# Optimization experiments

Measured on AMD Instinct MI355X. Metric: run time of the kernel, lower is better.

Reference implementation:

```python
import jax, jax.numpy as jnp
from jax import lax
import numpy as np

K = 2        # k-hop MIS / number of rw SpGEMM iterations
EPS = 0.5    # lazy random-walk epsilon
N = 2048     # nodes
D = 512      # feature dim
E = 65536    # edges (avg degree 32)


def setup_inputs() -> dict:
    key = jax.random.key(0)
    k1, k2, k3, k4 = jax.random.split(key, 4)
    edge_index = jax.random.randint(k1, (2, E), 0, N, dtype=jnp.int32)
    edge_attr = jax.random.uniform(k2, (E,), dtype=jnp.float32)
    x = jax.random.normal(k3, (N, D), dtype=jnp.float32)
    rank = jnp.arange(N, dtype=jnp.int32)  # node ordering ('random' ordering = some permutation; identity here)
    u = jax.random.uniform(k4, (N, N), dtype=jnp.float32)  # noise for row-wise multinomial sampling
    return {"edge_index": edge_index, "edge_attr": edge_attr, "x": x, "rank": rank, "u": u}


def _maximal_k_independent_set(row, col, rank, n, k):
    """Greedy maximal k-independent set: nodes that are local rank-minima within k hops."""
    big = jnp.int32(n)

    def prop_min(r):  # one hop of min-propagation (message row -> col), keep self
        return jnp.minimum(jax.ops.segment_min(r[row], col, num_segments=n), r)

    def prop_or(b):   # one hop of boolean OR propagation (as int32)
        return jnp.maximum(jax.ops.segment_max(b[row], col, num_segments=n), b)

    def cond(st):
        mis, mask, mr = st
        return ~jnp.all(mask)

    def body(st):
        mis, mask, mr = st
        for _ in range(k):
            mr = prop_min(mr)
        mis = mis | (rank == mr)
        mk = mis.astype(jnp.int32)
        for _ in range(k):
            mk = prop_or(mk)
        mask = mk > 0
        mr = jnp.where(mask, big, rank)
        return mis, mask, mr

    init = (jnp.zeros(n, bool), jnp.zeros(n, bool), rank)
    mis, _, _ = lax.while_loop(cond, body, init)
    return mis


def _row_normalize(m):
    s = m.sum(axis=1, keepdims=True)
    return m / jnp.where(s > 0, s, 1.0)


def reference(edge_index, edge_attr, x, rank, u):
    n = x.shape[0]
    row, col = edge_index[0], edge_index[1]

    # --- MIS over the graph structure (integer-only) ---
    mis = _maximal_k_independent_set(row, col, rank, n, K)

    # --- adjacency (dense padded form of the SparseTensor) ---
    adj = jnp.zeros((n, n), x.dtype).at[row, col].add(edge_attr)

    # --- lazy random walk: rw = D^-1 A, offdiag *= (1-eps), diag = old_diag + eps ---
    rw = _row_normalize(adj)
    di = jnp.arange(n)
    new_diag = rw[di, di] + EPS  # computed BEFORE scaling, per original code
    rw = (rw * (1.0 - EPS)).at[di, di].set(new_diag)

    # --- c_mat = rw^K @ eye[:, mis]; padded to [n, n] with zero non-MIS columns ---
    c = jnp.where(mis[None, :], jnp.eye(n, dtype=x.dtype), 0.0)
    for _ in range(K):
        c = rw @ c
    c = _row_normalize(c)

    # --- sample_partition_matrix: per-row multinomial via Gumbel-argmax ---
    g = -jnp.log(-jnp.log(u + 1e-20) + 1e-20)
    logits = jnp.where(c > 0, jnp.log(jnp.maximum(c, 1e-30)), -jnp.inf) + g
    cluster = jnp.argmax(logits, axis=1)                 # [n] cluster id (a MIS column)
    c_hard = jax.nn.one_hot(cluster, n, dtype=x.dtype)   # partition matrix [n, n]

    # --- p_inv = row-normalized c_hard.T ---
    counts = c_hard.sum(axis=0)
    p_inv = c_hard.T / jnp.where(counts > 0, counts, 1.0)[:, None]

    # --- coarsen: c^T A c, pool: p_inv @ x ---
    adj_c = c_hard.T @ adj @ c_hard
    x_pool = p_inv @ x
    return adj_c, c_hard, p_inv, mis, x_pool
```

## Files before the change

kernel.cpp:

```cpp
#include <hip/hip_runtime.h>
#include <hip/hip_bf16.h>
#include <math.h>
#include <stdint.h>

#define NN 2048
#define DD 512
#define EE 65536
#define EPSV 0.5f
#define SEN 2048
#define PADE 98304

static const size_t SZ = (size_t)NN * NN;

__global__ __launch_bounds__(256) void count_deg(const int* __restrict__ row,
                                                 const int* __restrict__ col,
                                                 int* __restrict__ degree,
                                                 int* __restrict__ cdeg) {
  int e = blockIdx.x * 256 + threadIdx.x;
  atomicAdd(&degree[row[e]], 1);
  atomicAdd(&cdeg[col[e]], 1);
}

__global__ __launch_bounds__(1024) void csr_scan_pad(const int* __restrict__ degree,
                                                     const int* __restrict__ cdeg,
                                                     int* __restrict__ row_ptr,
                                                     int* __restrict__ fill_ptr,
                                                     int* __restrict__ col_ptr,
                                                     int* __restrict__ cfill_ptr,
                                                     unsigned short* __restrict__ colidx,
                                                     unsigned short* __restrict__ rowidx,
                                                     float* __restrict__ avals,
                                                     unsigned long long* __restrict__ packed,
                                                     int* __restrict__ counts) {
  __shared__ int a[NN], b[NN], c[NN], d[NN];
  int t = threadIdx.x;
  for (int v = t; v < NN; v += 1024) {
    a[v] = (degree[v] + 15) & ~15;
    c[v] = (cdeg[v] + 15) & ~15;
    packed[v] = 0ull;
    counts[v] = 0;
  }
  __syncthreads();
  int* s1 = a; int* d1 = b; int* s2 = c; int* d2 = d;
  for (int off = 1; off < NN; off <<= 1) {
    for (int v = t; v < NN; v += 1024) {
      d1[v] = s1[v] + (v >= off ? s1[v - off] : 0);
      d2[v] = s2[v] + (v >= off ? s2[v - off] : 0);
    }
    __syncthreads();
    int* tp = s1; s1 = d1; d1 = tp;
    tp = s2; s2 = d2; d2 = tp;
  }
  for (int v = t; v < NN; v += 1024) {
    int dg = degree[v];
    int end = s1[v];
    int excl = end - ((dg + 15) & ~15);
    row_ptr[v] = excl;
    fill_ptr[v] = excl;
    for (int e = excl + dg; e < end; ++e) {
      colidx[e] = (unsigned short)v;
      avals[e] = 0.f;
    }
    dg = cdeg[v];
    end = s2[v];
    excl = end - ((dg + 15) & ~15);
    col_ptr[v] = excl;
    cfill_ptr[v] = excl;
    for (int e = excl + dg; e < end; ++e) rowidx[e] = (unsigned short)v;
  }
  if (t == 0) {
    row_ptr[NN] = s1[NN - 1];
    col_ptr[NN] = s2[NN - 1];
  }
}

__global__ __launch_bounds__(256) void csr_fill(const int* __restrict__ row,
                                                const int* __restrict__ col,
                                                const float* __restrict__ attr,
                                                int* __restrict__ fill_ptr,
                                                int* __restrict__ cfill_ptr,
                                                unsigned short* __restrict__ colidx,
                                                unsigned short* __restrict__ rowidx,
                                                float* __restrict__ avals) {
  int e = blockIdx.x * 256 + threadIdx.x;
  int r = row[e], c = col[e];
  int pos = atomicAdd(&fill_ptr[r], 1);
  colidx[pos] = (unsigned short)c;
  avals[pos] = attr[e];
  rowidx[atomicAdd(&cfill_ptr[c], 1)] = (unsigned short)r;
}

__global__ __launch_bounds__(1024) void mis_kernel(const int* __restrict__ row_ptr_g,
                                                   const int* __restrict__ col_ptr_g,
                                                   const unsigned short* __restrict__ colidx,
                                                   const unsigned short* __restrict__ rowidx,
                                                   const int* __restrict__ rank_g,
                                                   int* __restrict__ mis_flag,
                                                   int* __restrict__ mis_list,
                                                   int* __restrict__ misinv,
                                                   int* __restrict__ mis_count) {
  __shared__ int rank_s[NN];
  __shared__ int mr[NN];
  __shared__ int cov[NN];
  __shared__ int dly[NN];
  __shared__ int mis_s[NN];
  __shared__ int row_ptr_s[NN + 1];
  __shared__ int col_ptr_s[NN + 1];
  __shared__ int unc[2][NN];
  __shared__ int dl[NN];
  __shared__ int ucnt[2];
  __shared__ int dcnt;
  __shared__ int cnt;
  int t = threadIdx.x;
  const uint4* col4 = (const uint4*)colidx;
  const uint4* row4 = (const uint4*)rowidx;

  for (int v = t; v < NN; v += 1024) {
    int rk = rank_g[v];
    rank_s[v] = rk;
    mr[v] = rk;
    cov[v] = 0;
    dly[v] = 0;
    mis_s[v] = 0;
    row_ptr_s[v] = row_ptr_g[v];
    col_ptr_s[v] = col_ptr_g[v];
    unc[0][v] = v;
  }
  if (t == 0) {
    row_ptr_s[NN] = row_ptr_g[NN];
    col_ptr_s[NN] = col_ptr_g[NN];
    ucnt[0] = NN;
    ucnt[1] = 0;
    dcnt = 0;
    cnt = 0;
  }
  __syncthreads();

  int cur = 0;
  for (int round = 0; round < NN; ++round) {
    int U = ucnt[cur];
    if (round) {
      for (int v = t; v < NN; v += 1024) {
        mr[v] = cov[v] ? SEN : rank_s[v];
        dly[v] = 0;
      }
      if (t == 0) { ucnt[cur ^ 1] = 0; dcnt = 0; }
      __syncthreads();
    }
    for (int i = t; i < U; i += 1024) {
      int v = unc[cur][i];
      int val = rank_s[v];
      int e0 = row_ptr_s[v];
      int nch = (row_ptr_s[v + 1] - e0) >> 3;
      const uint4* b4 = col4 + (e0 >> 3);
      for (int cI = 0; cI < nch; cI += 2) {
        uint4 A = b4[cI], B = b4[cI + 1];
        atomicMin(&mr[A.x & 0xFFFFu], val); atomicMin(&mr[A.x >> 16], val);
        atomicMin(&mr[A.y & 0xFFFFu], val); atomicMin(&mr[A.y >> 16], val);
        atomicMin(&mr[A.z & 0xFFFFu], val); atomicMin(&mr[A.z >> 16], val);
        atomicMin(&mr[A.w & 0xFFFFu], val); atomicMin(&mr[A.w >> 16], val);
        atomicMin(&mr[B.x & 0xFFFFu], val); atomicMin(&mr[B.x >> 16], val);
        atomicMin(&mr[B.y & 0xFFFFu], val); atomicMin(&mr[B.y >> 16], val);
        atomicMin(&mr[B.z & 0xFFFFu], val); atomicMin(&mr[B.z >> 16], val);
        atomicMin(&mr[B.w & 0xFFFFu], val); atomicMin(&mr[B.w >> 16], val);
      }
    }
    __syncthreads();
    for (int i = t; i < U; i += 1024) {
      int v = unc[cur][i];
      int val = mr[v];
      int e0 = col_ptr_s[v];
      int nch = (col_ptr_s[v + 1] - e0) >> 3;
      const uint4* b4 = row4 + (e0 >> 3);
      for (int cI = 0; cI < nch; cI += 2) {
        uint4 A = b4[cI], B = b4[cI + 1];
        int m0 = min(mr[A.x & 0xFFFFu], mr[A.x >> 16]);
        int m1 = min(mr[A.y & 0xFFFFu], mr[A.y >> 16]);
        int m2 = min(mr[A.z & 0xFFFFu], mr[A.z >> 16]);
        int m3 = min(mr[A.w & 0xFFFFu], mr[A.w >> 16]);
        int m4 = min(mr[B.x & 0xFFFFu], mr[B.x >> 16]);
        int m5 = min(mr[B.y & 0xFFFFu], mr[B.y >> 16]);
        int m6 = min(mr[B.z & 0xFFFFu], mr[B.z >> 16]);
        int m7 = min(mr[B.w & 0xFFFFu], mr[B.w >> 16]);
        val = min(val, min(min(min(m0, m1), min(m2, m3)),
                           min(min(m4, m5), min(m6, m7))));
      }
      if (rank_s[v] == val) {
        mis_s[v] = 1;
        dly[v] = 1;
        dl[atomicAdd(&dcnt, 1)] = v;
      }
    }
    __syncthreads();
    int D = dcnt;
    for (int i = t; i < D; i += 1024) {
      int v = dl[i];
      int e0 = row_ptr_s[v];
      int nch = (row_ptr_s[v + 1] - e0) >> 3;
      const uint4* b4 = col4 + (e0 >> 3);
      for (int cI = 0; cI < nch; cI += 2) {
        uint4 A = b4[cI], B = b4[cI + 1];
        dly[A.x & 0xFFFFu] = 1; dly[A.x >> 16] = 1;
        dly[A.y & 0xFFFFu] = 1; dly[A.y >> 16] = 1;
        dly[A.z & 0xFFFFu] = 1; dly[A.z >> 16] = 1;
        dly[A.w & 0xFFFFu] = 1; dly[A.w >> 16] = 1;
        dly[B.x & 0xFFFFu] = 1; dly[B.x >> 16] = 1;
        dly[B.y & 0xFFFFu] = 1; dly[B.y >> 16] = 1;
        dly[B.z & 0xFFFFu] = 1; dly[B.z >> 16] = 1;
        dly[B.w & 0xFFFFu] = 1; dly[B.w >> 16] = 1;
      }
    }
    __syncthreads();
    for (int i = t; i < U; i += 1024) {
      int v = unc[cur][i];
      int c1 = dly[v];
      if (!c1) {
        int e0 = col_ptr_s[v];
        int nch = (col_ptr_s[v + 1] - e0) >> 3;
        const uint4* b4 = row4 + (e0 >> 3);
        for (int cI = 0; cI < nch; cI += 2) {
          uint4 A = b4[cI], B = b4[cI + 1];
          c1 |= dly[A.x & 0xFFFFu] | dly[A.x >> 16] |
                dly[A.y & 0xFFFFu] | dly[A.y >> 16] |
                dly[A.z & 0xFFFFu] | dly[A.z >> 16] |
                dly[A.w & 0xFFFFu] | dly[A.w >> 16] |
                dly[B.x & 0xFFFFu] | dly[B.x >> 16] |
                dly[B.y & 0xFFFFu] | dly[B.y >> 16] |
                dly[B.z & 0xFFFFu] | dly[B.z >> 16] |
                dly[B.w & 0xFFFFu] | dly[B.w >> 16];
          if (c1) break;
        }
      }
      if (c1) cov[v] = 1;
      else unc[cur ^ 1][atomicAdd(&ucnt[cur ^ 1], 1)] = v;
    }
    __syncthreads();
    if (ucnt[cur ^ 1] == 0) break;
    cur ^= 1;
  }

  for (int v = t; v < NN; v += 1024) {
    int s = mis_s[v];
    mis_flag[v] = s;
    int slot = -1;
    if (s) {
      slot = atomicAdd(&cnt, 1);
      mis_list[slot] = v;
    }
    misinv[v] = slot;
  }
  __syncthreads();
  if (t == 0) *mis_count = cnt;
}

__global__ __launch_bounds__(256) void rw_build(const int* __restrict__ row_ptr,
                                                const unsigned short* __restrict__ colidx,
                                                const float* __restrict__ avals,
                                                const int* __restrict__ misinv,
                                                float* __restrict__ rw,
                                                float* __restrict__ Bc) {
  int i = blockIdx.x;
  __shared__ float rowbuf[NN];
  __shared__ float ssum;
  int t = threadIdx.x;
  for (int j = t; j < NN; j += 256) rowbuf[j] = 0.f;
  if (t == 0) ssum = 0.f;
  __syncthreads();
  int e0 = row_ptr[i], e1 = row_ptr[i + 1];
  float part = 0.f;
  for (int e = e0 + t; e < e1; e += 256) {
    float a = avals[e];
    atomicAdd(&rowbuf[colidx[e]], a);
    part += a;
  }
  for (int off = 32; off; off >>= 1) part += __shfl_down(part, off);
  if ((t & 63) == 0) atomicAdd(&ssum, part);
  __syncthreads();
  float s = ssum;
  s = (s > 0.f) ? s : 1.f;
  for (int j = t; j < NN; j += 256) {
    float v = rowbuf[j] / s;
    v = (i == j) ? (v + EPSV) : (v * (1.f - EPSV));
    rw[(size_t)i * NN + j] = v;
    int tc = misinv[j];
    if (tc >= 0) Bc[(size_t)tc * NN + i] = v;
  }
}

__device__ inline unsigned int f32_key(float x) {
  unsigned int u = __float_as_uint(x);
  return (u & 0x80000000u) ? ~u : (u | 0x80000000u);
}
__device__ inline float dot4(float4 a, float4 b) {
  return ((a.x * b.x + a.y * b.y) + (a.z * b.z + a.w * b.w));
}
__device__ inline unsigned long long umax64(unsigned long long a, unsigned long long b) {
  return a > b ? a : b;
}
__device__ inline int pdecode(unsigned long long p) {
  return (p == 0ull) ? 0 : (NN - 1 - (int)(p & 0xFFFFFFFFull));
}

__global__ __launch_bounds__(256) void c2_argmax(const float* __restrict__ rw,
                                                 const float* __restrict__ Bc,
                                                 const float* __restrict__ u,
                                                 const int* __restrict__ mis_list,
                                                 const int* __restrict__ mis_count,
                                                 unsigned long long* __restrict__ packed) {
  int M = *mis_count;
  int ncg = (M + 3) >> 2;
  int njobs = ncg * 64;
  int lane = threadIdx.x & 63, w = threadIdx.x >> 6;
  for (int j = blockIdx.x; j < njobs; j += gridDim.x) {
    int cg = j >> 6, tile = j & 63;
    int c0 = cg * 4;
    float4 creg[4][8];
    int mcol[4];
#pragma unroll
    for (int cc = 0; cc < 4; ++cc) {
      int colv = c0 + cc;
      int cl = colv < M ? colv : (M - 1);
      mcol[cc] = mis_list[cl];
      const float4* cb = (const float4*)(Bc + (size_t)cl * NN);
#pragma unroll
      for (int q = 0; q < 8; ++q) creg[cc][q] = cb[q * 64 + lane];
    }
    int rbase = tile * 32 + w * 8;
#pragma unroll
    for (int it = 0; it < 8; ++it) {
      int r = rbase + it;
      const float4* rp = (const float4*)(rw + (size_t)r * NN);
      float4 a0 = rp[lane], a1 = rp[64 + lane], a2 = rp[128 + lane], a3 = rp[192 + lane];
      float4 a4 = rp[256 + lane], a5 = rp[320 + lane], a6 = rp[384 + lane], a7 = rp[448 + lane];
      float sacc[4];
#pragma unroll
      for (int cc = 0; cc < 4; ++cc) {
        float s01 = dot4(a0, creg[cc][0]) + dot4(a1, creg[cc][1]);
        float s23 = dot4(a2, creg[cc][2]) + dot4(a3, creg[cc][3]);
        float s45 = dot4(a4, creg[cc][4]) + dot4(a5, creg[cc][5]);
        float s67 = dot4(a6, creg[cc][6]) + dot4(a7, creg[cc][7]);
        float s = (s01 + s23) + (s45 + s67);
        s += __shfl_xor(s, 32);
        s += __shfl_xor(s, 16);
        s += __shfl_xor(s, 8);
        s += __shfl_xor(s, 4);
        s += __shfl_xor(s, 2);
        s += __shfl_xor(s, 1);
        sacc[cc] = s;
      }
      if (lane == 0) {
        unsigned long long best = 0ull;
#pragma unroll
        for (int cc = 0; cc < 4; ++cc) {
          if (c0 + cc < M && sacc[cc] > 0.f) {
            int m = mcol[cc];
            float uu = u[(size_t)r * NN + m];
            float g = -logf(-logf(uu + 1e-20f) + 1e-20f);
            float logit = logf(sacc[cc]) + g;
            unsigned long long key =
                ((unsigned long long)f32_key(logit) << 32) | (unsigned int)(NN - 1 - m);
            best = umax64(best, key);
          }
        }
        if (best) atomicMax(&packed[r], best);
      }
    }
  }
}

__global__ __launch_bounds__(256) void decode_zero(const unsigned long long* __restrict__ packed,
                                                   int* __restrict__ cluster,
                                                   int* __restrict__ counts,
                                                   float* __restrict__ adjc,
                                                   float* __restrict__ xp) {
  int idx = blockIdx.x * 256 + threadIdx.x;
  if (idx < (int)SZ) adjc[idx] = 0.f;
  else xp[idx - (int)SZ] = 0.f;
  if (idx < NN) {
    int m = pdecode(packed[idx]);
    cluster[idx] = m;
    atomicAdd(&counts[m], 1);
  }
}

__global__ __launch_bounds__(256) void scatter_chpm(const int* __restrict__ row,
                                                    const int* __restrict__ col,
                                                    const float* __restrict__ attr,
                                                    const float* __restrict__ x,
                                                    const int* __restrict__ cluster,
                                                    const int* __restrict__ counts,
                                                    const int* __restrict__ mis_flag,
                                                    float* __restrict__ out_ch,
                                                    float* __restrict__ out_pinv,
                                                    float* __restrict__ out_mis,
                                                    float* __restrict__ adjc,
                                                    float* __restrict__ xp) {
  int idx = blockIdx.x * 256 + threadIdx.x;
  int a = idx >> 11, b = idx & (NN - 1);
  out_ch[idx] = (cluster[a] == b) ? 1.f : 0.f;
  float pv = 0.f;
  if (cluster[b] == a) {
    int c = counts[a];
    pv = 1.f / (float)(c > 0 ? c : 1);
  }
  out_pinv[idx] = pv;
  if (idx < NN) out_mis[idx] = mis_flag[idx] ? 1.f : 0.f;
  if (idx < NN * DD) {
    int i = idx >> 9;
    int ci = cluster[i];
    int c = counts[ci];
    atomicAdd(&xp[ci * DD + (idx & (DD - 1))], x[idx] / (float)(c > 0 ? c : 1));
  }
  if (idx < EE) {
    atomicAdd(&adjc[(size_t)cluster[row[idx]] * NN + cluster[col[idx]]], attr[idx]);
  }
}

extern "C" void kernel_launch(void* const* d_in, const int* in_sizes, int n_in,
                              void* d_out, int out_size, void* d_ws, size_t ws_size,
                              hipStream_t stream) {
  const int*   edge_index = (const int*)d_in[0];
  const float* edge_attr  = (const float*)d_in[1];
  const float* x          = (const float*)d_in[2];
  const int*   rank       = (const int*)d_in[3];
  const float* u          = (const float*)d_in[4];
  float* out              = (float*)d_out;

  const int* row = edge_index;
  const int* col = edge_index + EE;

  float* out_adjc = out;
  float* out_ch   = out + SZ;
  float* out_pinv = out + 2 * SZ;
  float* out_mis  = out + 3 * SZ;
  float* out_xp   = out + 3 * SZ + NN;

  int*   degree    = (int*)d_ws;
  int*   cdeg      = degree + NN;
  unsigned long long* packed = (unsigned long long*)(cdeg + NN);
  int*   counts    = (int*)(packed + NN);
  int*   mis_flag  = counts + NN;
  int*   cluster   = mis_flag + NN;
  int*   mis_list  = cluster + NN;
  int*   misinv    = mis_list + NN;
  int*   mis_count = misinv + NN;
  int*   fill_ptr  = mis_count + 1;
  int*   cfill_ptr = fill_ptr + NN;
  int*   row_ptr   = cfill_ptr + NN;
  int*   col_ptr   = row_ptr + NN + 1;
  unsigned short* colidx =
      (unsigned short*)(((uintptr_t)(col_ptr + NN + 1) + 31) & ~(uintptr_t)31);
  unsigned short* rowidx = colidx + PADE;
  float* avals = (float*)(rowidx + PADE);

  hipMemsetAsync(d_ws, 0, 2 * NN * sizeof(int), stream);
  count_deg<<<EE / 256, 256, 0, stream>>>(row, col, degree, cdeg);
  csr_scan_pad<<<1, 1024, 0, stream>>>(degree, cdeg, row_ptr, fill_ptr, col_ptr,
                                       cfill_ptr, colidx, rowidx, avals, packed, counts);
  csr_fill<<<EE / 256, 256, 0, stream>>>(row, col, edge_attr, fill_ptr, cfill_ptr,
                                         colidx, rowidx, avals);
  mis_kernel<<<1, 1024, 0, stream>>>(row_ptr, col_ptr, colidx, rowidx, rank,
                                     mis_flag, mis_list, misinv, mis_count);
  rw_build<<<NN, 256, 0, stream>>>(row_ptr, colidx, avals, misinv, out_adjc, out_ch);
  c2_argmax<<<1024, 256, 0, stream>>>(out_adjc, out_ch, u, mis_list, mis_count, packed);
  decode_zero<<<(unsigned)((SZ + (size_t)NN * DD) / 256), 256, 0, stream>>>(
      packed, cluster, counts, out_adjc, out_xp);
  scatter_chpm<<<(NN * NN) / 256, 256, 0, stream>>>(row, col, edge_attr, x, cluster,
                                                    counts, mis_flag, out_ch, out_pinv,
                                                    out_mis, out_adjc, out_xp);
}
```

Baseline: 242.4 us.

## Overlap single-block MIS with rw construction in one fused launch

Merges the single-block MIS kernel and the per-row random-walk build into one launch: block 0 runs the MIS while the other blocks build rw rows and zero adjc/xp, so the serial MIS overlaps with bandwidth work. Because rw no longer knows the MIS mapping, the MIS-column gather into Bc moves to a new bc_gather kernel, and rw is staged in the pinv output buffer instead of adjc. The zeroing is taken out of decode, which shrinks to NN threads. The risk is that block 0 needs a lot of shared memory and may be scheduled late or slowed by the 1024-thread rw blocks around it.

```diff
diff --git a/kernel.cpp b/kernel.cpp
--- a/kernel.cpp
+++ b/kernel.cpp
@@ -90,200 +90,213 @@
   rowidx[atomicAdd(&cfill_ptr[c], 1)] = (unsigned short)r;
 }
 
-__global__ __launch_bounds__(1024) void mis_kernel(const int* __restrict__ row_ptr_g,
-                                                   const int* __restrict__ col_ptr_g,
-                                                   const unsigned short* __restrict__ colidx,
-                                                   const unsigned short* __restrict__ rowidx,
-                                                   const int* __restrict__ rank_g,
-                                                   int* __restrict__ mis_flag,
-                                                   int* __restrict__ mis_list,
-                                                   int* __restrict__ misinv,
-                                                   int* __restrict__ mis_count) {
-  __shared__ int rank_s[NN];
-  __shared__ int mr[NN];
-  __shared__ int cov[NN];
-  __shared__ int dly[NN];
-  __shared__ int mis_s[NN];
-  __shared__ int row_ptr_s[NN + 1];
-  __shared__ int col_ptr_s[NN + 1];
-  __shared__ int unc[2][NN];
-  __shared__ int dl[NN];
-  __shared__ int ucnt[2];
-  __shared__ int dcnt;
-  __shared__ int cnt;
-  int t = threadIdx.x;
-  const uint4* col4 = (const uint4*)colidx;
-  const uint4* row4 = (const uint4*)rowidx;
-
-  for (int v = t; v < NN; v += 1024) {
-    int rk = rank_g[v];
-    rank_s[v] = rk;
-    mr[v] = rk;
-    cov[v] = 0;
-    dly[v] = 0;
-    mis_s[v] = 0;
-    row_ptr_s[v] = row_ptr_g[v];
-    col_ptr_s[v] = col_ptr_g[v];
-    unc[0][v] = v;
-  }
-  if (t == 0) {
-    row_ptr_s[NN] = row_ptr_g[NN];
-    col_ptr_s[NN] = col_ptr_g[NN];
-    ucnt[0] = NN;
-    ucnt[1] = 0;
-    dcnt = 0;
-    cnt = 0;
-  }
-  __syncthreads();
-
-  int cur = 0;
-  for (int round = 0; round < NN; ++round) {
-    int U = ucnt[cur];
-    if (round) {
-      for (int v = t; v < NN; v += 1024) {
-        mr[v] = cov[v] ? SEN : rank_s[v];
-        dly[v] = 0;
-      }
-      if (t == 0) { ucnt[cur ^ 1] = 0; dcnt = 0; }
+__global__ __launch_bounds__(1024) void fused_mis_rw(const int* __restrict__ row_ptr_g,
+                                                     const int* __restrict__ col_ptr_g,
+                                                     const unsigned short* __restrict__ colidx,
+                                                     const unsigned short* __restrict__ rowidx,
+                                                     const int* __restrict__ rank_g,
+                                                     int* __restrict__ mis_flag,
+                                                     int* __restrict__ mis_list,
+                                                     int* __restrict__ misinv,
+                                                     int* __restrict__ mis_count,
+                                                     const float* __restrict__ avals,
+                                                     float* __restrict__ rw,
+                                                     float* __restrict__ adjc,
+                                                     float* __restrict__ xp) {
+  if (blockIdx.x == 0) {
+    __shared__ int rank_s[NN];
+    __shared__ int mr[NN];
+    __shared__ int cov[NN];
+    __shared__ int dly[NN];
+    __shared__ int mis_s[NN];
+    __shared__ int row_ptr_s[NN + 1];
+    __shared__ int col_ptr_s[NN + 1];
+    __shared__ int unc[2][NN];
+    __shared__ int dl[NN];
+    __shared__ int ucnt[2];
+    __shared__ int dcnt;
+    __shared__ int cnt;
+    int t = threadIdx.x;
+    const uint4* col4 = (const uint4*)colidx;
+    const uint4* row4 = (const uint4*)rowidx;
+
+    for (int v = t; v < NN; v += 1024) {
+      int rk = rank_g[v];
+      rank_s[v] = rk;
+      mr[v] = rk;
+      cov[v] = 0;
+      dly[v] = 0;
+      mis_s[v] = 0;
+      row_ptr_s[v] = row_ptr_g[v];
+      col_ptr_s[v] = col_ptr_g[v];
+      unc[0][v] = v;
+    }
+    if (t == 0) {
+      row_ptr_s[NN] = row_ptr_g[NN];
+      col_ptr_s[NN] = col_ptr_g[NN];
+      ucnt[0] = NN;
+      ucnt[1] = 0;
+      dcnt = 0;
+      cnt = 0;
+    }
+    __syncthreads();
+
+    int cur = 0;
+    for (int round = 0; round < NN; ++round) {
+      int U = ucnt[cur];
+      if (round) {
+        for (int v = t; v < NN; v += 1024) {
+          mr[v] = cov[v] ? SEN : rank_s[v];
+          dly[v] = 0;
+        }
+        if (t == 0) { ucnt[cur ^ 1] = 0; dcnt = 0; }
+        __syncthreads();
+      }
+      for (int i = t; i < U; i += 1024) {
+        int v = unc[cur][i];
+        int val = rank_s[v];
+        int e0 = row_ptr_s[v];
+        int nch = (row_ptr_s[v + 1] - e0) >> 3;
+        const uint4* b4 = col4 + (e0 >> 3);
+        for (int cI = 0; cI < nch; cI += 2) {
+          uint4 A = b4[cI], B = b4[cI + 1];
+          atomicMin(&mr[A.x & 0xFFFFu], val); atomicMin(&mr[A.x >> 16], val);
+          atomicMin(&mr[A.y & 0xFFFFu], val); atomicMin(&mr[A.y >> 16], val);
+          atomicMin(&mr[A.z & 0xFFFFu], val); atomicMin(&mr[A.z >> 16], val);
+          atomicMin(&mr[A.w & 0xFFFFu], val); atomicMin(&mr[A.w >> 16], val);
+          atomicMin(&mr[B.x & 0xFFFFu], val); atomicMin(&mr[B.x >> 16], val);
+          atomicMin(&mr[B.y & 0xFFFFu], val); atomicMin(&mr[B.y >> 16], val);
+          atomicMin(&mr[B.z & 0xFFFFu], val); atomicMin(&mr[B.z >> 16], val);
+          atomicMin(&mr[B.w & 0xFFFFu], val); atomicMin(&mr[B.w >> 16], val);
+        }
+      }
       __syncthreads();
-    }
-    for (int i = t; i < U; i += 1024) {
-      int v = unc[cur][i];
-      int val = rank_s[v];
-      int e0 = row_ptr_s[v];
-      int nch = (row_ptr_s[v + 1] - e0) >> 3;
-      const uint4* b4 = col4 + (e0 >> 3);
-      for (int cI = 0; cI < nch; cI += 2) {
-        uint4 A = b4[cI], B = b4[cI + 1];
-        atomicMin(&mr[A.x & 0xFFFFu], val); atomicMin(&mr[A.x >> 16], val);
-        atomicMin(&mr[A.y & 0xFFFFu], val); atomicMin(&mr[A.y >> 16], val);
-        atomicMin(&mr[A.z & 0xFFFFu], val); atomicMin(&mr[A.z >> 16], val);
-        atomicMin(&mr[A.w & 0xFFFFu], val); atomicMin(&mr[A.w >> 16], val);
-        atomicMin(&mr[B.x & 0xFFFFu], val); atomicMin(&mr[B.x >> 16], val);
-        atomicMin(&mr[B.y & 0xFFFFu], val); atomicMin(&mr[B.y >> 16], val);
-        atomicMin(&mr[B.z & 0xFFFFu], val); atomicMin(&mr[B.z >> 16], val);
-        atomicMin(&mr[B.w & 0xFFFFu], val); atomicMin(&mr[B.w >> 16], val);
-      }
-    }
-    __syncthreads();
-    for (int i = t; i < U; i += 1024) {
-      int v = unc[cur][i];
-      int val = mr[v];
-      int e0 = col_ptr_s[v];
-      int nch = (col_ptr_s[v + 1] - e0) >> 3;
-      const uint4* b4 = row4 + (e0 >> 3);
-      for (int cI = 0; cI < nch; cI += 2) {
-        uint4 A = b4[cI], B = b4[cI + 1];
-        int m0 = min(mr[A.x & 0xFFFFu], mr[A.x >> 16]);
-        int m1 = min(mr[A.y & 0xFFFFu], mr[A.y >> 16]);
-        int m2 = min(mr[A.z & 0xFFFFu], mr[A.z >> 16]);
-        int m3 = min(mr[A.w & 0xFFFFu], mr[A.w >> 16]);
-        int m4 = min(mr[B.x & 0xFFFFu], mr[B.x >> 16]);
-        int m5 = min(mr[B.y & 0xFFFFu], mr[B.y >> 16]);
-        int m6 = min(mr[B.z & 0xFFFFu], mr[B.z >> 16]);
-        int m7 = min(mr[B.w & 0xFFFFu], mr[B.w >> 16]);
-        val = min(val, min(min(min(m0, m1), min(m2, m3)),
-                           min(min(m4, m5), min(m6, m7))));
-      }
-      if (rank_s[v] == val) {
-        mis_s[v] = 1;
-        dly[v] = 1;
-        dl[atomicAdd(&dcnt, 1)] = v;
-      }
-    }
-    __syncthreads();
-    int D = dcnt;
-    for (int i = t; i < D; i += 1024) {
-      int v = dl[i];
-      int e0 = row_ptr_s[v];
-      int nch = (row_ptr_s[v + 1] - e0) >> 3;
-      const uint4* b4 = col4 + (e0 >> 3);
-      for (int cI = 0; cI < nch; cI += 2) {
-        uint4 A = b4[cI], B = b4[cI + 1];
-        dly[A.x & 0xFFFFu] = 1; dly[A.x >> 16] = 1;
-        dly[A.y & 0xFFFFu] = 1; dly[A.y >> 16] = 1;
-        dly[A.z & 0xFFFFu] = 1; dly[A.z >> 16] = 1;
-        dly[A.w & 0xFFFFu] = 1; dly[A.w >> 16] = 1;
-        dly[B.x & 0xFFFFu] = 1; dly[B.x >> 16] = 1;
-        dly[B.y & 0xFFFFu] = 1; dly[B.y >> 16] = 1;
-        dly[B.z & 0xFFFFu] = 1; dly[B.z >> 16] = 1;
-        dly[B.w & 0xFFFFu] = 1; dly[B.w >> 16] = 1;
-      }
-    }
-    __syncthreads();
-    for (int i = t; i < U; i += 1024) {
-      int v = unc[cur][i];
-      int c1 = dly[v];
-      if (!c1) {
+      for (int i = t; i < U; i += 1024) {
+        int v = unc[cur][i];
+        int val = mr[v];
         int e0 = col_ptr_s[v];
         int nch = (col_ptr_s[v + 1] - e0) >> 3;
         const uint4* b4 = row4 + (e0 >> 3);
         for (int cI = 0; cI < nch; cI += 2) {
           uint4 A = b4[cI], B = b4[cI + 1];
-          c1 |= dly[A.x & 0xFFFFu] | dly[A.x >> 16] |
-                dly[A.y & 0xFFFFu] | dly[A.y >> 16] |
-                dly[A.z & 0xFFFFu] | dly[A.z >> 16] |
-                dly[A.w & 0xFFFFu] | dly[A.w >> 16] |
-                dly[B.x & 0xFFFFu] | dly[B.x >> 16] |
-                dly[B.y & 0xFFFFu] | dly[B.y >> 16] |
-                dly[B.z & 0xFFFFu] | dly[B.z >> 16] |
-                dly[B.w & 0xFFFFu] | dly[B.w >> 16];
-          if (c1) break;
-        }
-      }
-      if (c1) cov[v] = 1;
-      else unc[cur ^ 1][atomicAdd(&ucnt[cur ^ 1], 1)] = v;
+          int m0 = min(mr[A.x & 0xFFFFu], mr[A.x >> 16]);
+          int m1 = min(mr[A.y & 0xFFFFu], mr[A.y >> 16]);
+          int m2 = min(mr[A.z & 0xFFFFu], mr[A.z >> 16]);
+          int m3 = min(mr[A.w & 0xFFFFu], mr[A.w >> 16]);
+          int m4 = min(mr[B.x & 0xFFFFu], mr[B.x >> 16]);
+          int m5 = min(mr[B.y & 0xFFFFu], mr[B.y >> 16]);
+          int m6 = min(mr[B.z & 0xFFFFu], mr[B.z >> 16]);
+          int m7 = min(mr[B.w & 0xFFFFu], mr[B.w >> 16]);
+          val = min(val, min(min(min(m0, m1), min(m2, m3)),
+                             min(min(m4, m5), min(m6, m7))));
+        }
+        if (rank_s[v] == val) {
+          mis_s[v] = 1;
+          dly[v] = 1;
+          dl[atomicAdd(&dcnt, 1)] = v;
+        }
+      }
+      __syncthreads();
+      int D = dcnt;
+      for (int i = t; i < D; i += 1024) {
+        int v = dl[i];
+        int e0 = row_ptr_s[v];
+        int nch = (row_ptr_s[v + 1] - e0) >> 3;
+        const uint4* b4 = col4 + (e0 >> 3);
+        for (int cI = 0; cI < nch; cI += 2) {
+          uint4 A = b4[cI], B = b4[cI + 1];
+          dly[A.x & 0xFFFFu] = 1; dly[A.x >> 16] = 1;
+          dly[A.y & 0xFFFFu] = 1; dly[A.y >> 16] = 1;
+          dly[A.z & 0xFFFFu] = 1; dly[A.z >> 16] = 1;
+          dly[A.w & 0xFFFFu] = 1; dly[A.w >> 16] = 1;
+          dly[B.x & 0xFFFFu] = 1; dly[B.x >> 16] = 1;
+          dly[B.y & 0xFFFFu] = 1; dly[B.y >> 16] = 1;
+          dly[B.z & 0xFFFFu] = 1; dly[B.z >> 16] = 1;
+          dly[B.w & 0xFFFFu] = 1; dly[B.w >> 16] = 1;
+        }
+      }
+      __syncthreads();
+      for (int i = t; i < U; i += 1024) {
+        int v = unc[cur][i];
+        int c1 = dly[v];
+        if (!c1) {
+          int e0 = col_ptr_s[v];
+          int nch = (col_ptr_s[v + 1] - e0) >> 3;
+          const uint4* b4 = row4 + (e0 >> 3);
+          for (int cI = 0; cI < nch; cI += 2) {
+            uint4 A = b4[cI], B = b4[cI + 1];
+            c1 |= dly[A.x & 0xFFFFu] | dly[A.x >> 16] |
+                  dly[A.y & 0xFFFFu] | dly[A.y >> 16] |
+                  dly[A.z & 0xFFFFu] | dly[A.z >> 16] |
+                  dly[A.w & 0xFFFFu] | dly[A.w >> 16] |
+                  dly[B.x & 0xFFFFu] | dly[B.x >> 16] |
+                  dly[B.y & 0xFFFFu] | dly[B.y >> 16] |
+                  dly[B.z & 0xFFFFu] | dly[B.z >> 16] |
+                  dly[B.w & 0xFFFFu] | dly[B.w >> 16];
+            if (c1) break;
+          }
+        }
+        if (c1) cov[v] = 1;
+        else unc[cur ^ 1][atomicAdd(&ucnt[cur ^ 1], 1)] = v;
+      }
+      __syncthreads();
+      if (ucnt[cur ^ 1] == 0) break;
+      cur ^= 1;
+    }
+
+    for (int v = t; v < NN; v += 1024) {
+      int s = mis_s[v];
+      mis_flag[v] = s;
+      int slot = -1;
+      if (s) {
+        slot = atomicAdd(&cnt, 1);
+        mis_list[slot] = v;
+      }
+      misinv[v] = slot;
     }
     __syncthreads();
-    if (ucnt[cur ^ 1] == 0) break;
-    cur ^= 1;
-  }
-
-  for (int v = t; v < NN; v += 1024) {
-    int s = mis_s[v];
-    mis_flag[v] = s;
-    int slot = -1;
-    if (s) {
-      slot = atomicAdd(&cnt, 1);
-      mis_list[slot] = v;
-    }
-    misinv[v] = slot;
-  }
-  __syncthreads();
-  if (t == 0) *mis_count = cnt;
-}
-
-__global__ __launch_bounds__(256) void rw_build(const int* __restrict__ row_ptr,
-                                                const unsigned short* __restrict__ colidx,
-                                                const float* __restrict__ avals,
-                                                const int* __restrict__ misinv,
-                                                float* __restrict__ rw,
-                                                float* __restrict__ Bc) {
-  int i = blockIdx.x;
-  __shared__ float rowbuf[NN];
-  __shared__ float ssum;
-  int t = threadIdx.x;
-  for (int j = t; j < NN; j += 256) rowbuf[j] = 0.f;
-  if (t == 0) ssum = 0.f;
-  __syncthreads();
-  int e0 = row_ptr[i], e1 = row_ptr[i + 1];
-  float part = 0.f;
-  for (int e = e0 + t; e < e1; e += 256) {
-    float a = avals[e];
-    atomicAdd(&rowbuf[colidx[e]], a);
-    part += a;
-  }
-  for (int off = 32; off; off >>= 1) part += __shfl_down(part, off);
-  if ((t & 63) == 0) atomicAdd(&ssum, part);
-  __syncthreads();
-  float s = ssum;
-  s = (s > 0.f) ? s : 1.f;
-  for (int j = t; j < NN; j += 256) {
-    float v = rowbuf[j] / s;
-    v = (i == j) ? (v + EPSV) : (v * (1.f - EPSV));
-    rw[(size_t)i * NN + j] = v;
-    int tc = misinv[j];
-    if (tc >= 0) Bc[(size_t)tc * NN + i] = v;
+    if (t == 0) *mis_count = cnt;
+  } else {
+    __shared__ float rowbuf[NN];
+    __shared__ float ssum;
+    int i = blockIdx.x - 1;
+    int t = threadIdx.x;
+    float4 z4 = make_float4(0.f, 0.f, 0.f, 0.f);
+    if (t < 512) ((float4*)(adjc + (size_t)i * NN))[t] = z4;
+    if (t < 128) ((float4*)xp)[(size_t)i * 128 + t] = z4;
+    for (int j = t; j < NN; j += 1024) rowbuf[j] = 0.f;
+    if (t == 0) ssum = 0.f;
+    __syncthreads();
+    int e0 = row_ptr_g[i], e1 = row_ptr_g[i + 1];
+    float part = 0.f;
+    for (int e = e0 + t; e < e1; e += 1024) {
+      float a = avals[e];
+      atomicAdd(&rowbuf[colidx[e]], a);
+      part += a;
+    }
+    for (int off = 32; off; off >>= 1) part += __shfl_down(part, off);
+    if ((t & 63) == 0) atomicAdd(&ssum, part);
+    __syncthreads();
+    float s = ssum;
+    s = (s > 0.f) ? s : 1.f;
+    for (int j = t; j < NN; j += 1024) {
+      float v = rowbuf[j] / s;
+      v = (i == j) ? (v + EPSV) : (v * (1.f - EPSV));
+      rw[(size_t)i * NN + j] = v;
+    }
+  }
+}
+
+__global__ __launch_bounds__(256) void bc_gather(const float* __restrict__ rw,
+                                                 const int* __restrict__ mis_list,
+                                                 const int* __restrict__ mis_count,
+                                                 float* __restrict__ Bc) {
+  int M = *mis_count;
+  int total = M * NN;
+  int stride = gridDim.x * 256;
+  for (int j = blockIdx.x * 256 + threadIdx.x; j < total; j += stride) {
+    int tc = j >> 11, i = j & (NN - 1);
+    Bc[(size_t)tc * NN + i] = rw[(size_t)i * NN + mis_list[tc]];
   }
 }
 
@@ -368,19 +381,13 @@
   }
 }
 
-__global__ __launch_bounds__(256) void decode_zero(const unsigned long long* __restrict__ packed,
-                                                   int* __restrict__ cluster,
-                                                   int* __restrict__ counts,
-                                                   float* __restrict__ adjc,
-                                                   float* __restrict__ xp) {
+__global__ __launch_bounds__(256) void decode_cnt(const unsigned long long* __restrict__ packed,
+                                                  int* __restrict__ cluster,
+                                                  int* __restrict__ counts) {
   int idx = blockIdx.x * 256 + threadIdx.x;
-  if (idx < (int)SZ) adjc[idx] = 0.f;
-  else xp[idx - (int)SZ] = 0.f;
-  if (idx < NN) {
-    int m = pdecode(packed[idx]);
-    cluster[idx] = m;
-    atomicAdd(&counts[m], 1);
-  }
+  int m = pdecode(packed[idx]);
+  cluster[idx] = m;
+  atomicAdd(&counts[m], 1);
 }
 
 __global__ __launch_bounds__(256) void scatter_chpm(const int* __restrict__ row,
@@ -459,12 +466,12 @@
                                        cfill_ptr, colidx, rowidx, avals, packed, counts);
   csr_fill<<<EE / 256, 256, 0, stream>>>(row, col, edge_attr, fill_ptr, cfill_ptr,
                                          colidx, rowidx, avals);
-  mis_kernel<<<1, 1024, 0, stream>>>(row_ptr, col_ptr, colidx, rowidx, rank,
-                                     mis_flag, mis_list, misinv, mis_count);
-  rw_build<<<NN, 256, 0, stream>>>(row_ptr, colidx, avals, misinv, out_adjc, out_ch);
-  c2_argmax<<<1024, 256, 0, stream>>>(out_adjc, out_ch, u, mis_list, mis_count, packed);
-  decode_zero<<<(unsigned)((SZ + (size_t)NN * DD) / 256), 256, 0, stream>>>(
-      packed, cluster, counts, out_adjc, out_xp);
+  fused_mis_rw<<<NN + 1, 1024, 0, stream>>>(row_ptr, col_ptr, colidx, rowidx, rank,
+                                            mis_flag, mis_list, misinv, mis_count,
+                                            avals, out_pinv , out_adjc, out_xp);
+  bc_gather<<<256, 256, 0, stream>>>(out_pinv, mis_list, mis_count, out_ch);
+  c2_argmax<<<1024, 256, 0, stream>>>(out_pinv, out_ch, u, mis_list, mis_count, packed);
+  decode_cnt<<<NN / 256, 256, 0, stream>>>(packed, cluster, counts);
   scatter_chpm<<<(NN * NN) / 256, 256, 0, stream>>>(row, col, edge_attr, x, cluster,
                                                     counts, mis_flag, out_ch, out_pinv,
                                                     out_mis, out_adjc, out_xp);
```

After: 234.6 us. -3.2%, faster.
